# Optimization experiments

Hardware: AMD Instinct MI355X
Metric: run time of the kernel (lower is better)

## Reference

```python
import jax, jax.numpy as jnp
import numpy as np


def setup_inputs() -> dict:
    key = jax.random.key(0)
    x = jax.random.uniform(key, (16, 1024, 512), dtype=jnp.float32)
    return {"x": x, "n_bits": 10}


def reference(x, n_bits):
    # Successive-approximation binary encoding: bit i fires if the residual
    # signal exceeds 2^-(i+1); residual is reduced by that threshold when it fires.
    v = jnp.clip(x, 0.0, 1.0)  # [B, T, C]
    bits = []
    decision = 0.5
    for _ in range(n_bits):
        s = (v >= decision).astype(x.dtype)
        bits.append(s)
        v = v - s * decision
        decision = decision * 0.5
    # stack along new bit axis -> [B, T, n_bits, C]
    return jnp.stack(bits, axis=2)
```

## Files before the change

### kernel.cpp

```cpp
#include <hip/hip_runtime.h>


#define C_DIM 512
#define C4    128

typedef float f32x4 __attribute__((ext_vector_type(4)));

__global__ __launch_bounds__(256) void binenc_kernel(const float* __restrict__ x,
                                                     const int* __restrict__ n_bits_p,
                                                     float* __restrict__ out) {
    const int n_bits = *n_bits_p;
    const float scale = (float)(1u << n_bits);
    const int   maxq  = (1 << n_bits) - 1;

    const int row  = blockIdx.x;
    const int tid  = threadIdx.x;
    const int c4   = tid & (C4 - 1);
    const int bit0 = tid >> 7;

    const f32x4 xv = reinterpret_cast<const f32x4*>(x)[row * C4 + c4];

    int q[4];
#pragma unroll
    for (int j = 0; j < 4; ++j) {
        float v  = fminf(fmaxf(xv[j], 0.0f), 1.0f);
        int   qi = (int)(v * scale);
        q[j] = qi > maxq ? maxq : qi;
    }

    f32x4* rowbase = reinterpret_cast<f32x4*>(out) + (size_t)row * n_bits * C4;
#pragma unroll 5
    for (int k = 0; 2 * k + bit0 < n_bits; ++k) {
        const int sh = n_bits - 1 - (2 * k + bit0);
        f32x4 s;
#pragma unroll
        for (int j = 0; j < 4; ++j)
            s[j] = (float)((q[j] >> sh) & 1);
        rowbase[k * 256 + tid] = s;
    }
}

extern "C" void kernel_launch(void* const* d_in, const int* in_sizes, int n_in,
                              void* d_out, int out_size, void* d_ws, size_t ws_size,
                              hipStream_t stream) {
    const float* x        = (const float*)d_in[0];
    const int*   n_bits_p = (const int*)d_in[1];
    float*       out      = (float*)d_out;

    const int n_rows = in_sizes[0] / C_DIM;
    const int block  = 256;

    binenc_kernel<<<n_rows, block, 0, stream>>>(x, n_bits_p, out);
}
```

Before: 73.23 us.

## Split encoding into pack-to-u16 and expand kernels using workspace

Adds a first kernel that quantizes the input into 16-bit codes stored in workspace, and a second kernel that expands those codes into float bits. The aim is to halve the input bytes the expand kernel reads per row. The cost is an extra kernel launch and an extra workspace write and read. When workspace is too small, the original fused kernel is used instead.

```diff
diff --git a/kernel.cpp b/kernel.cpp
--- a/kernel.cpp
+++ b/kernel.cpp
@@ -4,11 +4,58 @@
 #define C_DIM 512
 #define C4    128
 
-typedef float f32x4 __attribute__((ext_vector_type(4)));
+typedef float  f32x4 __attribute__((ext_vector_type(4)));
+typedef unsigned short u16;
+typedef u16    u16x4 __attribute__((ext_vector_type(4)));
 
-__global__ __launch_bounds__(256) void binenc_kernel(const float* __restrict__ x,
+__global__ __launch_bounds__(256) void binenc_pack(const float* __restrict__ x,
+                                                   const int* __restrict__ n_bits_p,
+                                                   u16* __restrict__ codes,
+                                                   int n_vec) {
+    const int n_bits = *n_bits_p;
+    const float scale = (float)(1u << n_bits);
+    const int   maxq  = (1 << n_bits) - 1;
+
+    const int vid = blockIdx.x * blockDim.x + threadIdx.x;
+    if (vid >= n_vec) return;
+
+    const f32x4 xv = reinterpret_cast<const f32x4*>(x)[vid];
+    u16x4 c;
+#pragma unroll
+    for (int j = 0; j < 4; ++j) {
+        float v  = fminf(fmaxf(xv[j], 0.0f), 1.0f);
+        int   qi = (int)(v * scale);
+        c[j] = (u16)(qi > maxq ? maxq : qi);
+    }
+    reinterpret_cast<u16x4*>(codes)[vid] = c;
+}
+
+__global__ __launch_bounds__(256) void binenc_expand(const u16* __restrict__ codes,
                                                      const int* __restrict__ n_bits_p,
                                                      float* __restrict__ out) {
+    const int n_bits = *n_bits_p;
+    const int row  = blockIdx.x;
+    const int tid  = threadIdx.x;
+    const int c4   = tid & (C4 - 1);
+    const int bit0 = tid >> 7;
+
+    const u16x4 q = reinterpret_cast<const u16x4*>(codes)[row * C4 + c4];
+
+    f32x4* rowbase = reinterpret_cast<f32x4*>(out) + (size_t)row * n_bits * C4;
+#pragma unroll 5
+    for (int k = 0; 2 * k + bit0 < n_bits; ++k) {
+        const int sh = n_bits - 1 - (2 * k + bit0);
+        f32x4 s;
+#pragma unroll
+        for (int j = 0; j < 4; ++j)
+            s[j] = (float)((q[j] >> sh) & 1);
+        rowbase[k * 256 + tid] = s;
+    }
+}
+
+__global__ __launch_bounds__(256) void binenc_fused(const float* __restrict__ x,
+                                                    const int* __restrict__ n_bits_p,
+                                                    float* __restrict__ out) {
     const int n_bits = *n_bits_p;
     const float scale = (float)(1u << n_bits);
     const int   maxq  = (1 << n_bits) - 1;
@@ -19,7 +66,6 @@
     const int bit0 = tid >> 7;
 
     const f32x4 xv = reinterpret_cast<const f32x4*>(x)[row * C4 + c4];
-
     int q[4];
 #pragma unroll
     for (int j = 0; j < 4; ++j) {
@@ -47,8 +93,16 @@
     const int*   n_bits_p = (const int*)d_in[1];
     float*       out      = (float*)d_out;
 
-    const int n_rows = in_sizes[0] / C_DIM;
-    const int block  = 256;
+    const int n_elems = in_sizes[0];
+    const int n_rows  = n_elems / C_DIM;
+    const int block   = 256;
 
-    binenc_kernel<<<n_rows, block, 0, stream>>>(x, n_bits_p, out);
+    if (ws_size >= (size_t)n_elems * sizeof(u16)) {
+        u16* codes = (u16*)d_ws;
+        const int n_vec = n_elems >> 2;
+        binenc_pack<<<(n_vec + block - 1) / block, block, 0, stream>>>(x, n_bits_p, codes, n_vec);
+        binenc_expand<<<n_rows, block, 0, stream>>>(codes, n_bits_p, out);
+    } else {
+        binenc_fused<<<n_rows, block, 0, stream>>>(x, n_bits_p, out);
+    }
 }
```

Result: slower. 77.56 us (+5.9%).
